# Kernel tuning notes

Measured on AMD Instinct MI355X. Metric: run time of the kernel, lower is better.

The kernel has to match this reference:

```python
import jax, jax.numpy as jnp
import numpy as np

B, C, H, W = 4, 64, 64, 64  # prompt and kv share the same BCHW shape
EPS = 1e-5
OFR = 4.0  # offset_range_factor
SCALE = (C // 1) ** -0.5  # n_head_channels = dim / n_heads = 64


def conv1x1(x, w, b=None):
    y = jnp.einsum('oc,bchw->bohw', w, x)
    if b is not None:
        y = y + b[None, :, None, None]
    return y


def grid_sample_bilinear(img, grid):
    # img: [N,C,Hp,Wp], grid: [N,Hg,Wg,2] with (x,y) in [-1,1], align_corners=True, zeros padding
    N, Cc, Hp, Wp = img.shape
    Hg, Wg = grid.shape[1], grid.shape[2]
    gx = (grid[..., 0] + 1.0) * 0.5 * (Wp - 1)
    gy = (grid[..., 1] + 1.0) * 0.5 * (Hp - 1)
    x0 = jnp.floor(gx)
    y0 = jnp.floor(gy)
    img_f = img.reshape(N, Cc, Hp * Wp)

    def gather(xi, yi):
        valid = (xi >= 0) & (xi <= Wp - 1) & (yi >= 0) & (yi <= Hp - 1)
        xi_c = jnp.clip(xi, 0, Wp - 1).astype(jnp.int32)
        yi_c = jnp.clip(yi, 0, Hp - 1).astype(jnp.int32)
        idx = (yi_c * Wp + xi_c).reshape(N, 1, -1)
        vals = jnp.take_along_axis(img_f, idx, axis=2)  # [N,C,Hg*Wg]
        return vals, valid.reshape(N, 1, -1).astype(img.dtype)

    v00, m00 = gather(x0, y0)
    v01, m01 = gather(x0 + 1, y0)
    v10, m10 = gather(x0, y0 + 1)
    v11, m11 = gather(x0 + 1, y0 + 1)
    wx = (gx - x0).reshape(N, 1, -1)
    wy = (gy - y0).reshape(N, 1, -1)
    out = (v00 * m00 * (1 - wx) * (1 - wy) + v01 * m01 * wx * (1 - wy)
           + v10 * m10 * (1 - wx) * wy + v11 * m11 * wx * wy)
    return out.reshape(N, Cc, Hg, Wg)


def setup_inputs() -> dict:
    key = jax.random.key(0)
    ks = jax.random.split(key, 8)
    s = 0.02
    return {
        'prompt': jax.random.normal(ks[0], (B, C, H, W), jnp.float32),
        'kv': jax.random.normal(ks[1], (B, C, H, W), jnp.float32),
        'wq': s * jax.random.normal(ks[2], (C, C), jnp.float32),
        'bq': jnp.zeros((C,), jnp.float32),
        'wk': s * jax.random.normal(ks[3], (C, C), jnp.float32),
        'bk': jnp.zeros((C,), jnp.float32),
        'wv': s * jax.random.normal(ks[4], (C, C), jnp.float32),
        'bv': jnp.zeros((C,), jnp.float32),
        'wo': s * jax.random.normal(ks[5], (C, C), jnp.float32),
        'bo': jnp.zeros((C,), jnp.float32),
        'dw_w': s * jax.random.normal(ks[6], (C, 1, 3, 3), jnp.float32),  # depthwise 3x3
        'dw_b': jnp.zeros((C,), jnp.float32),
        'ln_w': jnp.ones((C,), jnp.float32),
        'ln_b': jnp.zeros((C,), jnp.float32),
        'off_w': s * jax.random.normal(ks[7], (2, C), jnp.float32),  # 1x1 conv to 2 offset channels
    }


def reference(prompt, kv, wq, bq, wk, bk, wv, bv, wo, bo, dw_w, dw_b, ln_w, ln_b, off_w):
    # q projection (n_groups=1 so group view == full view)
    q = conv1x1(prompt, wq, bq)  # [B,C,H,W]

    # conv_offset: depthwise 3x3 -> WithBias LayerNorm over channels -> GELU -> 1x1 to 2ch
    t = jax.lax.conv_general_dilated(q, dw_w, (1, 1), ((1, 1), (1, 1)),
                                     feature_group_count=C)
    t = t + dw_b[None, :, None, None]
    mu = t.mean(axis=1, keepdims=True)
    var = t.var(axis=1, keepdims=True)
    t = (t - mu) / jnp.sqrt(var + EPS) * ln_w[None, :, None, None] + ln_b[None, :, None, None]
    t = jax.nn.gelu(t, approximate=False)
    offset = jnp.einsum('oc,bchw->bohw', off_w, t)  # [B,2,H,W] (y,x) channels

    Hk, Wk = offset.shape[2], offset.shape[3]
    n = Hk * Wk
    rng = jnp.array([1.0 / (Hk - 1.0), 1.0 / (Wk - 1.0)], dtype=offset.dtype).reshape(1, 2, 1, 1)
    offset = jnp.tanh(offset) * rng * OFR
    offset = jnp.transpose(offset, (0, 2, 3, 1))  # [B,Hk,Wk,2] (y,x)

    ref_y = (jnp.linspace(0.5, Hk - 0.5, Hk) / (Hk - 1.0)) * 2.0 - 1.0
    ref_x = (jnp.linspace(0.5, Wk - 0.5, Wk) / (Wk - 1.0)) * 2.0 - 1.0
    ry, rx = jnp.meshgrid(ref_y, ref_x, indexing='ij')
    ref = jnp.stack((ry, rx), axis=-1)[None].astype(offset.dtype)  # [1,Hk,Wk,2]

    pos = offset + ref
    grid = pos[..., ::-1]  # swap to (x,y)
    xs = grid_sample_bilinear(kv, grid)  # [B,C,Hk,Wk]
    xs = xs.reshape(B, C, n)

    k = jnp.einsum('oc,bcn->bon', wk, xs) + bk[None, :, None]
    v = jnp.einsum('oc,bcn->bon', wv, xs) + bv[None, :, None]
    qf = q.reshape(B, C, H * W)

    attn = jnp.einsum('bcm,bcn->bmn', qf, k) * SCALE  # [B,HW,n]
    attn = jax.nn.softmax(attn, axis=2)
    out = jnp.einsum('bmn,bcn->bcm', attn, v).reshape(B, C, H, W)
    return conv1x1(out, wo, bo)
```

## Files before the change

kernel.cpp:

```cpp
#include <hip/hip_runtime.h>
#include <math.h>

#define BB 4
#define CC 64
#define HH 64
#define WW 64
#define HWP 4096
#define NPTS 4096
#define LDP 72
constexpr float K_EPS   = 1e-5f;
constexpr float K_OFR   = 4.0f;
constexpr float K_QSCALE = 0.18033688011112042f;


typedef short frag8 __attribute__((ext_vector_type(8)));
typedef float f32x4 __attribute__((ext_vector_type(4)));

static __device__ inline unsigned short f2bf(float f) {
  unsigned int u = __builtin_bit_cast(unsigned int, f);
  unsigned int r = (u + 0x7fffu + ((u >> 16) & 1u)) >> 16;
  return (unsigned short)r;
}

#if defined(__has_builtin)
#if __has_builtin(__builtin_amdgcn_cvt_pk_bf16_f32)
#define HAVE_CVT_PK_BF16 1
#endif
#if __has_builtin(__builtin_amdgcn_exp2f)
#define EXP2F(x) __builtin_amdgcn_exp2f(x)
#endif
#endif
#ifndef EXP2F
#define EXP2F(x) exp2f(x)
#endif

static __device__ inline int pack2bf(float a, float b) {
#ifdef HAVE_CVT_PK_BF16
  auto r = __builtin_amdgcn_cvt_pk_bf16_f32(a, b);
  return __builtin_bit_cast(int, r);
#else
  return (int)f2bf(a) | ((int)f2bf(b) << 16);
#endif
}

__global__ __launch_bounds__(1024) void k_qproj(
    const float* __restrict__ prompt, const float* __restrict__ wq,
    const float* __restrict__ bq, float* __restrict__ qf,
    unsigned short* __restrict__ qb) {
  __shared__ float w_s[64 * 64];
  __shared__ float p_s[64 * 64];
  __shared__ unsigned short t_s[64 * 68];
  int tid = threadIdx.x;
  int blk = blockIdx.x;
  int b = blk >> 6; int hw0 = (blk & 63) * 64;
#pragma unroll
  for (int i = 0; i < 4; ++i) w_s[i * 1024 + tid] = wq[i * 1024 + tid];
#pragma unroll
  for (int i = 0; i < 4; ++i) {
    int idx = i * 1024 + tid; int c = idx >> 6, pix = idx & 63;
    p_s[idx] = prompt[(size_t)(b * CC + c) * HWP + hw0 + pix];
  }
  __syncthreads();
  int x = tid & 63, og = tid >> 6;
  float acc[4];
#pragma unroll
  for (int oo = 0; oo < 4; ++oo) acc[oo] = bq[og * 4 + oo];
  for (int cg = 0; cg < 16; ++cg) {
    float p0 = p_s[(cg * 4 + 0) * 64 + x];
    float p1 = p_s[(cg * 4 + 1) * 64 + x];
    float p2 = p_s[(cg * 4 + 2) * 64 + x];
    float p3 = p_s[(cg * 4 + 3) * 64 + x];
#pragma unroll
    for (int oo = 0; oo < 4; ++oo) {
      const float4 w4 = *(const float4*)&w_s[(og * 4 + oo) * 64 + cg * 4];
      acc[oo] = fmaf(w4.x, p0, fmaf(w4.y, p1, fmaf(w4.z, p2, fmaf(w4.w, p3, acc[oo]))));
    }
  }
#pragma unroll
  for (int oo = 0; oo < 4; ++oo) {
    int o = og * 4 + oo;
    qf[(size_t)(b * CC + o) * HWP + hw0 + x] = acc[oo];
    t_s[x * 68 + o] = f2bf(acc[oo] * K_QSCALE);
  }
  __syncthreads();
  {
    int pix = tid >> 4, c4 = tid & 15;
    ushort4 v = *(const ushort4*)&t_s[pix * 68 + c4 * 4];
    *(ushort4*)&qb[(size_t)(b * HWP + hw0 + pix) * CC + c4 * 4] = v;
  }
}

__global__ __launch_bounds__(1024) void k_off_sample(
    const float* __restrict__ q, const float* __restrict__ dw_w,
    const float* __restrict__ dw_b, const float* __restrict__ ln_w,
    const float* __restrict__ ln_b, const float* __restrict__ off_w,
    const float* __restrict__ kv,
    const float* __restrict__ wk, const float* __restrict__ bk,
    const float* __restrict__ wv, const float* __restrict__ bv,
    unsigned short* __restrict__ kb, unsigned short* __restrict__ vb) {
  __shared__ float wk_s[64 * 64];
  __shared__ float wv_s[64 * 64];
  __shared__ float xs_s[64 * 64];
  __shared__ float red0[16][64];
  __shared__ float red1[16][64];

  int tid = threadIdx.x;
  int x = tid & 63;
  int cg = tid >> 6;
  int by = blockIdx.x;
  int b = by >> 6;
  int y = by & 63;

#pragma unroll
  for (int i = 0; i < 4; ++i) {
    wk_s[i * 1024 + tid] = wk[i * 1024 + tid];
    wv_s[i * 1024 + tid] = wv[i * 1024 + tid];
  }

  float t[4];
#pragma unroll
  for (int i = 0; i < 4; ++i) {
    int c = cg * 4 + i;
    float acc = dw_b[c];
    const float* qc = q + (size_t)(b * CC + c) * HWP;
#pragma unroll
    for (int ky = 0; ky < 3; ++ky) {
      int yy = y + ky - 1;
      bool yok = (yy >= 0) && (yy < HH);
#pragma unroll
      for (int kx = 0; kx < 3; ++kx) {
        int xx = x + kx - 1;
        bool ok = yok && (xx >= 0) && (xx < WW);
        float v = ok ? qc[yy * WW + xx] : 0.f;
        acc = fmaf(dw_w[c * 9 + ky * 3 + kx], v, acc);
      }
    }
    t[i] = acc;
  }
  float s1 = 0.f, s2 = 0.f;
#pragma unroll
  for (int i = 0; i < 4; ++i) { s1 += t[i]; s2 += t[i] * t[i]; }
  red0[cg][x] = s1;
  red1[cg][x] = s2;
  __syncthreads();
  float mu = 0.f, ms = 0.f;
#pragma unroll
  for (int g = 0; g < 16; ++g) { mu += red0[g][x]; ms += red1[g][x]; }
  mu *= (1.f / 64.f); ms *= (1.f / 64.f);
  float rstd = rsqrtf(ms - mu * mu + K_EPS);

  float oy = 0.f, ox = 0.f;
#pragma unroll
  for (int i = 0; i < 4; ++i) {
    int c = cg * 4 + i;
    float g = (t[i] - mu) * rstd * ln_w[c] + ln_b[c];
    g = 0.5f * g * (1.f + erff(g * 0.70710678118654752f));
    oy = fmaf(off_w[c], g, oy);
    ox = fmaf(off_w[CC + c], g, ox);
  }
  __syncthreads();
  red0[cg][x] = oy;
  red1[cg][x] = ox;
  __syncthreads();
  if (cg == 0) {
    float osy = 0.f, osx = 0.f;
#pragma unroll
    for (int g = 0; g < 16; ++g) { osy += red0[g][x]; osx += red1[g][x]; }
    osy = tanhf(osy) * (K_OFR / (HH - 1));
    osx = tanhf(osx) * (K_OFR / (WW - 1));
    float ry = (y + 0.5f) * (2.f / 63.f) - 1.f;
    float rx = (x + 0.5f) * (2.f / 63.f) - 1.f;
    red0[0][x] = (osx + rx + 1.f) * 0.5f * (WW - 1);
    red0[1][x] = (osy + ry + 1.f) * 0.5f * (HH - 1);
  }
  __syncthreads();

  int n = x, og = cg;
  int n0 = y * 64;
  float gx = red0[0][n], gy = red0[1][n];
  float x0f = floorf(gx), y0f = floorf(gy);
  float wx = gx - x0f, wy = gy - y0f;
  int x0 = (int)x0f, y0 = (int)y0f;
  int x1 = x0 + 1, y1 = y0 + 1;
  float m00 = (x0 >= 0 && x0 < WW && y0 >= 0 && y0 < HH) ? 1.f : 0.f;
  float m01 = (x1 >= 0 && x1 < WW && y0 >= 0 && y0 < HH) ? 1.f : 0.f;
  float m10 = (x0 >= 0 && x0 < WW && y1 >= 0 && y1 < HH) ? 1.f : 0.f;
  float m11 = (x1 >= 0 && x1 < WW && y1 >= 0 && y1 < HH) ? 1.f : 0.f;
  int x0c = min(max(x0, 0), WW - 1), x1c = min(max(x1, 0), WW - 1);
  int y0c = min(max(y0, 0), HH - 1), y1c = min(max(y1, 0), HH - 1);
  int i00 = y0c * WW + x0c, i01 = y0c * WW + x1c;
  int i10 = y1c * WW + x0c, i11 = y1c * WW + x1c;
  float w00 = m00 * (1.f - wx) * (1.f - wy);
  float w01 = m01 * wx * (1.f - wy);
  float w10 = m10 * (1.f - wx) * wy;
  float w11 = m11 * wx * wy;

  const float* base = kv + (size_t)b * CC * HWP;
#pragma unroll
  for (int i = 0; i < 4; ++i) {
    int c = og * 4 + i;
    const float* pc = base + (size_t)c * HWP;
    xs_s[c * 64 + n] = w00 * pc[i00] + w01 * pc[i01] + w10 * pc[i10] + w11 * pc[i11];
  }
  __syncthreads();
  float ak[4], av[4];
#pragma unroll
  for (int oo = 0; oo < 4; ++oo) { ak[oo] = bk[og * 4 + oo]; av[oo] = bv[og * 4 + oo]; }
  for (int cg2 = 0; cg2 < 16; ++cg2) {
    float p0 = xs_s[(cg2 * 4 + 0) * 64 + n];
    float p1 = xs_s[(cg2 * 4 + 1) * 64 + n];
    float p2 = xs_s[(cg2 * 4 + 2) * 64 + n];
    float p3 = xs_s[(cg2 * 4 + 3) * 64 + n];
#pragma unroll
    for (int oo = 0; oo < 4; ++oo) {
      int o = og * 4 + oo;
      const float4 k4 = *(const float4*)&wk_s[o * 64 + cg2 * 4];
      const float4 v4 = *(const float4*)&wv_s[o * 64 + cg2 * 4];
      ak[oo] = fmaf(k4.x, p0, fmaf(k4.y, p1, fmaf(k4.z, p2, fmaf(k4.w, p3, ak[oo]))));
      av[oo] = fmaf(v4.x, p0, fmaf(v4.y, p1, fmaf(v4.z, p2, fmaf(v4.w, p3, av[oo]))));
    }
  }
  int2 kk;
  kk.x = pack2bf(ak[0], ak[1]);
  kk.y = pack2bf(ak[2], ak[3]);
  size_t krow = (size_t)(b * NPTS + n0 + n) * CC + og * 4;
  *(int2*)&kb[krow] = kk;
#pragma unroll
  for (int oo = 0; oo < 4; ++oo) {
    int o = og * 4 + oo;
    vb[(size_t)(b * CC + o) * NPTS + n0 + n] = f2bf(av[oo]);
  }
}

__global__ __launch_bounds__(256) void k_attn(
    const unsigned short* __restrict__ qb, const unsigned short* __restrict__ kb,
    const unsigned short* __restrict__ vb, float* __restrict__ opart,
    float* __restrict__ dpart, int ns_shift) {
  __shared__ short qp_s[64 * LDP];
  __shared__ short k_s[64 * LDP];
  __shared__ short v_s[64 * LDP];

  int tid = threadIdx.x;
  int w = tid >> 6, lane = tid & 63, quad = lane >> 4, l16 = lane & 15;
  int blk = blockIdx.x;
  int pair = blk & ((BB << ns_shift) - 1);
  int mt = blk >> (2 + ns_shift);
  int ns = pair & ((1 << ns_shift) - 1);
  int b = pair >> ns_shift;
  int m0 = mt * 64;

  const unsigned short* qbb = qb + (size_t)b * HWP * CC;
  const unsigned short* kbb = kb + (size_t)b * NPTS * CC;
  const unsigned short* vbb = vb + (size_t)b * CC * NPTS;

#pragma unroll
  for (int pass = 0; pass < 2; ++pass) {
    int idx = pass * 256 + tid;
    int row = idx >> 3, part = idx & 7;
    uint4 d = *(const uint4*)(qbb + (size_t)(m0 + row) * CC + part * 8);
    *(uint4*)&qp_s[row * LDP + part * 8] = d;
  }
  __syncthreads();
  frag8 a_frag[2];
#pragma unroll
  for (int kc = 0; kc < 2; ++kc)
    a_frag[kc] = *(const frag8*)&qp_s[(w * 16 + l16) * LDP + kc * 32 + quad * 8];

  frag8 ones;
#pragma unroll
  for (int i = 0; i < 8; ++i) ones[i] = (short)0x3F80;

  f32x4 o_acc[4];
  f32x4 d4;
  const f32x4 zz = {0.f, 0.f, 0.f, 0.f};
#pragma unroll
  for (int i = 0; i < 4; ++i) o_acc[i] = zz;
  d4 = zz;

  int niters = (NPTS / 64) >> ns_shift;
  int nbase = ns * niters * 64;
  for (int it = 0; it < niters; ++it) {
    int n0 = nbase + it * 64;
    __syncthreads();
#pragma unroll
    for (int pass = 0; pass < 2; ++pass) {
      int idx = pass * 256 + tid;
      int row = idx >> 3, part = idx & 7;
      uint4 dk = *(const uint4*)(kbb + (size_t)(n0 + row) * CC + part * 8);
      uint4 dv = *(const uint4*)(vbb + (size_t)row * NPTS + n0 + part * 8);
      *(uint4*)&k_s[row * LDP + part * 8] = dk;
      *(uint4*)&v_s[row * LDP + part * 8] = dv;
    }
    __syncthreads();

    f32x4 sT[4];
#pragma unroll
    for (int t = 0; t < 4; ++t) {
      frag8 kf = *(const frag8*)&k_s[(t * 16 + l16) * LDP + quad * 8];
      sT[t] = __builtin_amdgcn_mfma_f32_16x16x32_bf16(kf, a_frag[0], zz, 0, 0, 0);
    }
#pragma unroll
    for (int t = 0; t < 4; ++t) {
      frag8 kf = *(const frag8*)&k_s[(t * 16 + l16) * LDP + 32 + quad * 8];
      sT[t] = __builtin_amdgcn_mfma_f32_16x16x32_bf16(kf, a_frag[1], sT[t], 0, 0, 0);
    }
#pragma unroll
    for (int t = 0; t < 4; ++t) {
      int base_sh = (w * 16 + l16) * LDP + t * 16 + quad * 4;
      int p01 = pack2bf(EXP2F(sT[t][0]), EXP2F(sT[t][1]));
      int p23 = pack2bf(EXP2F(sT[t][2]), EXP2F(sT[t][3]));
      *(int*)&qp_s[base_sh]     = p01;
      *(int*)&qp_s[base_sh + 2] = p23;
    }
#pragma unroll
    for (int kc = 0; kc < 2; ++kc) {
      frag8 bp = *(const frag8*)&qp_s[(w * 16 + l16) * LDP + kc * 32 + quad * 8];
      d4 = __builtin_amdgcn_mfma_f32_16x16x32_bf16(ones, bp, d4, 0, 0, 0);
#pragma unroll
      for (int ct = 0; ct < 4; ++ct) {
        frag8 av = *(const frag8*)&v_s[(ct * 16 + l16) * LDP + kc * 32 + quad * 8];
        o_acc[ct] = __builtin_amdgcn_mfma_f32_16x16x32_bf16(av, bp, o_acc[ct], 0, 0, 0);
      }
    }
  }

  float* op = opart + (size_t)((ns * BB + b) * HWP + m0 + w * 16 + l16) * CC;
#pragma unroll
  for (int ct = 0; ct < 4; ++ct) {
    float4 o4;
    o4.x = o_acc[ct][0]; o4.y = o_acc[ct][1]; o4.z = o_acc[ct][2]; o4.w = o_acc[ct][3];
    *(float4*)&op[ct * 16 + quad * 4] = o4;
  }
  if (lane < 16)
    dpart[(ns * BB + b) * HWP + m0 + w * 16 + lane] = d4[0];
}

__global__ __launch_bounds__(256) void k_out(
    const float* __restrict__ opart, const float* __restrict__ dpart,
    const float* __restrict__ wo, const float* __restrict__ bo,
    float* __restrict__ out, int NS) {
  __shared__ float wo_s[CC * CC];
  __shared__ float t_s[32 * 65];
  int tid = threadIdx.x;
  int blk = blockIdx.x;
  int b = blk >> 7, mt = blk & 127, m0 = mt * 32;
  for (int i = tid; i < CC * CC; i += 256) wo_s[i] = wo[i];

#pragma unroll
  for (int it = 0; it < 8; ++it) {
    int idx = it * 256 + tid;
    int m = idx >> 6, c = idx & 63;
    float o = 0.f, d = 0.f;
    for (int s = 0; s < NS; ++s) {
      o += opart[(size_t)((s * BB + b) * HWP + m0 + m) * CC + c];
      d += dpart[(s * BB + b) * HWP + m0 + m];
    }
    t_s[m * 65 + c] = o / d;
  }
  __syncthreads();
  int ml = tid & 31, og = tid >> 5;
  for (int oo = 0; oo < 8; ++oo) {
    int o = og * 8 + oo;
    float acc = bo[o];
#pragma unroll
    for (int c = 0; c < 64; ++c) acc = fmaf(wo_s[o * CC + c], t_s[ml * 65 + c], acc);
    out[(size_t)(b * CC + o) * HWP + m0 + ml] = acc;
  }
}

extern "C" void kernel_launch(void* const* d_in, const int* in_sizes, int n_in,
                              void* d_out, int out_size, void* d_ws, size_t ws_size,
                              hipStream_t stream) {
  const float* prompt = (const float*)d_in[0];
  const float* kv     = (const float*)d_in[1];
  const float* wq     = (const float*)d_in[2];
  const float* bq     = (const float*)d_in[3];
  const float* wk     = (const float*)d_in[4];
  const float* bk     = (const float*)d_in[5];
  const float* wv     = (const float*)d_in[6];
  const float* bv     = (const float*)d_in[7];
  const float* wo     = (const float*)d_in[8];
  const float* bo     = (const float*)d_in[9];
  const float* dw_w   = (const float*)d_in[10];
  const float* dw_b   = (const float*)d_in[11];
  const float* ln_w   = (const float*)d_in[12];
  const float* ln_b   = (const float*)d_in[13];
  const float* off_w  = (const float*)d_in[14];
  float* out = (float*)d_out;
  float* ws  = (float*)d_ws;

  auto need = [](int ns) {
    return (size_t)((size_t)ns * 1048576 + 3 * 524288 + (size_t)ns * 16384) * sizeof(float);
  };
  int NS, ns_shift;
  if      (ws_size >= need(8)) { NS = 8; ns_shift = 3; }
  else if (ws_size >= need(4)) { NS = 4; ns_shift = 2; }
  else                         { NS = 2; ns_shift = 1; }

  float* opart          = ws;
  float* qf             = ws;
  unsigned short* qb    = (unsigned short*)(ws + (size_t)NS * 1048576);
  unsigned short* kb    = (unsigned short*)(ws + (size_t)NS * 1048576 + 524288);
  unsigned short* vb    = (unsigned short*)(ws + (size_t)NS * 1048576 + 2 * 524288);
  float* dpart          = ws + (size_t)NS * 1048576 + 3 * 524288;

  hipLaunchKernelGGL(k_qproj, dim3(BB * 64), dim3(1024), 0, stream,
                     prompt, wq, bq, qf, qb);
  hipLaunchKernelGGL(k_off_sample, dim3(BB * HH), dim3(1024), 0, stream,
                     qf, dw_w, dw_b, ln_w, ln_b, off_w,
                     kv, wk, bk, wv, bv, kb, vb);
  hipLaunchKernelGGL(k_attn, dim3(BB * NS * 64), dim3(256), 0, stream,
                     qb, kb, vb, opart, dpart, ns_shift);
  hipLaunchKernelGGL(k_out, dim3(BB * 128), dim3(256), 0, stream,
                     opart, dpart, wo, bo, out, NS);
}
```

Measured before the change: 168.8 us.

## Fuse q projection into offset/sampling kernel with halo-row recompute

Merges the q-projection kernel into the offset/sampling kernel. Each block recomputes the q projection for its row plus the two neighbouring rows in shared memory, so the depthwise 3x3 conv reads q from LDS instead of a global fp32 q buffer. This removes one launch and the global round trip of q, at the cost of about three times the q-projection arithmetic and more shared-memory reuse. It also replaces erff in GELU with a polynomial approximation using fast exp2, which lowers precision slightly.

```diff
diff --git a/kernel.cpp b/kernel.cpp
--- a/kernel.cpp
+++ b/kernel.cpp
@@ -43,141 +43,156 @@
 #endif
 }
 
-__global__ __launch_bounds__(1024) void k_qproj(
+static __device__ inline float erf_fast(float z) {
+  float s = (z < 0.f) ? -1.f : 1.f;
+  float a = fabsf(z);
+  float t = 1.f / fmaf(0.3275911f, a, 1.f);
+  float p = t * fmaf(t, fmaf(t, fmaf(t, fmaf(t, 1.061405429f, -1.453152027f),
+                                     1.421413741f), -0.284496736f), 0.254829592f);
+  float e = EXP2F(-a * a * 1.4426950408889634f);
+  return s * (1.f - p * e);
+}
+
+__global__ __launch_bounds__(1024) void k_prep(
     const float* __restrict__ prompt, const float* __restrict__ wq,
-    const float* __restrict__ bq, float* __restrict__ qf,
-    unsigned short* __restrict__ qb) {
-  __shared__ float w_s[64 * 64];
-  __shared__ float p_s[64 * 64];
-  __shared__ unsigned short t_s[64 * 68];
-  int tid = threadIdx.x;
-  int blk = blockIdx.x;
-  int b = blk >> 6; int hw0 = (blk & 63) * 64;
-#pragma unroll
-  for (int i = 0; i < 4; ++i) w_s[i * 1024 + tid] = wq[i * 1024 + tid];
-#pragma unroll
-  for (int i = 0; i < 4; ++i) {
-    int idx = i * 1024 + tid; int c = idx >> 6, pix = idx & 63;
-    p_s[idx] = prompt[(size_t)(b * CC + c) * HWP + hw0 + pix];
-  }
-  __syncthreads();
-  int x = tid & 63, og = tid >> 6;
-  float acc[4];
-#pragma unroll
-  for (int oo = 0; oo < 4; ++oo) acc[oo] = bq[og * 4 + oo];
-  for (int cg = 0; cg < 16; ++cg) {
-    float p0 = p_s[(cg * 4 + 0) * 64 + x];
-    float p1 = p_s[(cg * 4 + 1) * 64 + x];
-    float p2 = p_s[(cg * 4 + 2) * 64 + x];
-    float p3 = p_s[(cg * 4 + 3) * 64 + x];
-#pragma unroll
-    for (int oo = 0; oo < 4; ++oo) {
-      const float4 w4 = *(const float4*)&w_s[(og * 4 + oo) * 64 + cg * 4];
-      acc[oo] = fmaf(w4.x, p0, fmaf(w4.y, p1, fmaf(w4.z, p2, fmaf(w4.w, p3, acc[oo]))));
-    }
-  }
-#pragma unroll
-  for (int oo = 0; oo < 4; ++oo) {
-    int o = og * 4 + oo;
-    qf[(size_t)(b * CC + o) * HWP + hw0 + x] = acc[oo];
-    t_s[x * 68 + o] = f2bf(acc[oo] * K_QSCALE);
-  }
-  __syncthreads();
-  {
-    int pix = tid >> 4, c4 = tid & 15;
-    ushort4 v = *(const ushort4*)&t_s[pix * 68 + c4 * 4];
-    *(ushort4*)&qb[(size_t)(b * HWP + hw0 + pix) * CC + c4 * 4] = v;
-  }
-}
-
-__global__ __launch_bounds__(1024) void k_off_sample(
-    const float* __restrict__ q, const float* __restrict__ dw_w,
-    const float* __restrict__ dw_b, const float* __restrict__ ln_w,
-    const float* __restrict__ ln_b, const float* __restrict__ off_w,
-    const float* __restrict__ kv,
+    const float* __restrict__ bq,
+    const float* __restrict__ dw_w, const float* __restrict__ dw_b,
+    const float* __restrict__ ln_w, const float* __restrict__ ln_b,
+    const float* __restrict__ off_w, const float* __restrict__ kv,
     const float* __restrict__ wk, const float* __restrict__ bk,
     const float* __restrict__ wv, const float* __restrict__ bv,
-    unsigned short* __restrict__ kb, unsigned short* __restrict__ vb) {
-  __shared__ float wk_s[64 * 64];
-  __shared__ float wv_s[64 * 64];
-  __shared__ float xs_s[64 * 64];
-  __shared__ float red0[16][64];
-  __shared__ float red1[16][64];
-
+    unsigned short* __restrict__ qb, unsigned short* __restrict__ kb,
+    unsigned short* __restrict__ vb) {
+  __shared__ float buf[16384];
+  float* w_s = buf;
+  float* pq  = buf + 4096;
   int tid = threadIdx.x;
-  int x = tid & 63;
-  int cg = tid >> 6;
-  int by = blockIdx.x;
-  int b = by >> 6;
-  int y = by & 63;
-
+  int x = tid & 63, og = tid >> 6;
+  int by = blockIdx.x; int b = by >> 6, y = by & 63;
+
+#pragma unroll
+  for (int i = 0; i < 4; ++i) w_s[i * 1024 + tid] = wq[i * 1024 + tid];
+#pragma unroll
+  for (int i = 0; i < 12; ++i) {
+    int idx = i * 1024 + tid;
+    int j = idx >> 6, xx = idx & 63;
+    int c = j / 3, r = j - c * 3;
+    int ry = min(max(y + r - 1, 0), HH - 1);
+    pq[idx] = prompt[(size_t)(b * CC + c) * HWP + ry * WW + xx];
+  }
+  __syncthreads();
+
+  float qreg[3][4];
+#pragma unroll
+  for (int r = 0; r < 3; ++r)
+#pragma unroll
+    for (int oo = 0; oo < 4; ++oo) qreg[r][oo] = bq[og * 4 + oo];
+  for (int cg = 0; cg < 16; ++cg) {
+    float4 w4[4];
+#pragma unroll
+    for (int oo = 0; oo < 4; ++oo)
+      w4[oo] = *(const float4*)&w_s[(og * 4 + oo) * 64 + cg * 4];
+#pragma unroll
+    for (int r = 0; r < 3; ++r) {
+      float p0 = pq[(cg * 4 + 0) * 192 + r * 64 + x];
+      float p1 = pq[(cg * 4 + 1) * 192 + r * 64 + x];
+      float p2 = pq[(cg * 4 + 2) * 192 + r * 64 + x];
+      float p3 = pq[(cg * 4 + 3) * 192 + r * 64 + x];
+#pragma unroll
+      for (int oo = 0; oo < 4; ++oo)
+        qreg[r][oo] = fmaf(w4[oo].x, p0, fmaf(w4[oo].y, p1,
+                      fmaf(w4[oo].z, p2, fmaf(w4[oo].w, p3, qreg[r][oo]))));
+    }
+  }
+  __syncthreads();
+
+#pragma unroll
+  for (int r = 0; r < 3; ++r)
+#pragma unroll
+    for (int oo = 0; oo < 4; ++oo)
+      pq[(og * 4 + oo) * 192 + r * 64 + x] = qreg[r][oo];
+  {
+    int2 qq;
+    qq.x = pack2bf(qreg[1][0] * K_QSCALE, qreg[1][1] * K_QSCALE);
+    qq.y = pack2bf(qreg[1][2] * K_QSCALE, qreg[1][3] * K_QSCALE);
+    *(int2*)&qb[(size_t)(b * HWP + y * WW + x) * CC + og * 4] = qq;
+  }
+  __syncthreads();
+
+  float t[4];
+#pragma unroll
+  for (int i = 0; i < 4; ++i) {
+    int c = og * 4 + i;
+    float acc = dw_b[c];
+#pragma unroll
+    for (int ky = 0; ky < 3; ++ky) {
+      int yy = y + ky - 1;
+      bool yok = (yy >= 0) && (yy < HH);
+#pragma unroll
+      for (int kx = 0; kx < 3; ++kx) {
+        int xx = x + kx - 1;
+        bool ok = yok && (xx >= 0) && (xx < WW);
+        int xc = min(max(xx, 0), WW - 1);
+        float v = ok ? pq[c * 192 + ky * 64 + xc] : 0.f;
+        acc = fmaf(dw_w[c * 9 + ky * 3 + kx], v, acc);
+      }
+    }
+    t[i] = acc;
+  }
+  __syncthreads();
+
+  float* wk_s = pq;
+  float* wv_s = pq + 4096;
+  float* xs_s = pq + 8192;
 #pragma unroll
   for (int i = 0; i < 4; ++i) {
     wk_s[i * 1024 + tid] = wk[i * 1024 + tid];
     wv_s[i * 1024 + tid] = wv[i * 1024 + tid];
   }
 
-  float t[4];
-#pragma unroll
-  for (int i = 0; i < 4; ++i) {
-    int c = cg * 4 + i;
-    float acc = dw_b[c];
-    const float* qc = q + (size_t)(b * CC + c) * HWP;
-#pragma unroll
-    for (int ky = 0; ky < 3; ++ky) {
-      int yy = y + ky - 1;
-      bool yok = (yy >= 0) && (yy < HH);
-#pragma unroll
-      for (int kx = 0; kx < 3; ++kx) {
-        int xx = x + kx - 1;
-        bool ok = yok && (xx >= 0) && (xx < WW);
-        float v = ok ? qc[yy * WW + xx] : 0.f;
-        acc = fmaf(dw_w[c * 9 + ky * 3 + kx], v, acc);
-      }
-    }
-    t[i] = acc;
-  }
+  float* red0 = w_s;
+  float* red1 = w_s + 1024;
   float s1 = 0.f, s2 = 0.f;
 #pragma unroll
   for (int i = 0; i < 4; ++i) { s1 += t[i]; s2 += t[i] * t[i]; }
-  red0[cg][x] = s1;
-  red1[cg][x] = s2;
+  red0[og * 64 + x] = s1;
+  red1[og * 64 + x] = s2;
   __syncthreads();
   float mu = 0.f, ms = 0.f;
 #pragma unroll
-  for (int g = 0; g < 16; ++g) { mu += red0[g][x]; ms += red1[g][x]; }
+  for (int g = 0; g < 16; ++g) { mu += red0[g * 64 + x]; ms += red1[g * 64 + x]; }
   mu *= (1.f / 64.f); ms *= (1.f / 64.f);
   float rstd = rsqrtf(ms - mu * mu + K_EPS);
 
   float oy = 0.f, ox = 0.f;
 #pragma unroll
   for (int i = 0; i < 4; ++i) {
-    int c = cg * 4 + i;
+    int c = og * 4 + i;
     float g = (t[i] - mu) * rstd * ln_w[c] + ln_b[c];
-    g = 0.5f * g * (1.f + erff(g * 0.70710678118654752f));
+    g = 0.5f * g * (1.f + erf_fast(g * 0.70710678118654752f));
     oy = fmaf(off_w[c], g, oy);
     ox = fmaf(off_w[CC + c], g, ox);
   }
   __syncthreads();
-  red0[cg][x] = oy;
-  red1[cg][x] = ox;
-  __syncthreads();
-  if (cg == 0) {
+  red0[og * 64 + x] = oy;
+  red1[og * 64 + x] = ox;
+  __syncthreads();
+  if (og == 0) {
     float osy = 0.f, osx = 0.f;
 #pragma unroll
-    for (int g = 0; g < 16; ++g) { osy += red0[g][x]; osx += red1[g][x]; }
+    for (int g = 0; g < 16; ++g) { osy += red0[g * 64 + x]; osx += red1[g * 64 + x]; }
     osy = tanhf(osy) * (K_OFR / (HH - 1));
     osx = tanhf(osx) * (K_OFR / (WW - 1));
     float ry = (y + 0.5f) * (2.f / 63.f) - 1.f;
     float rx = (x + 0.5f) * (2.f / 63.f) - 1.f;
-    red0[0][x] = (osx + rx + 1.f) * 0.5f * (WW - 1);
-    red0[1][x] = (osy + ry + 1.f) * 0.5f * (HH - 1);
-  }
-  __syncthreads();
-
-  int n = x, og = cg;
+    w_s[2048 + x] = (osx + rx + 1.f) * 0.5f * (WW - 1);
+    w_s[2112 + x] = (osy + ry + 1.f) * 0.5f * (HH - 1);
+  }
+  __syncthreads();
+
+  int n = x;
   int n0 = y * 64;
-  float gx = red0[0][n], gy = red0[1][n];
+  float gx = w_s[2048 + n], gy = w_s[2112 + n];
   float x0f = floorf(gx), y0f = floorf(gy);
   float wx = gx - x0f, wy = gy - y0f;
   int x0 = (int)x0f, y0 = (int)y0f;
@@ -203,6 +218,7 @@
     xs_s[c * 64 + n] = w00 * pc[i00] + w01 * pc[i01] + w10 * pc[i10] + w11 * pc[i11];
   }
   __syncthreads();
+
   float ak[4], av[4];
 #pragma unroll
   for (int oo = 0; oo < 4; ++oo) { ak[oo] = bk[og * 4 + oo]; av[oo] = bv[og * 4 + oo]; }
@@ -223,8 +239,7 @@
   int2 kk;
   kk.x = pack2bf(ak[0], ak[1]);
   kk.y = pack2bf(ak[2], ak[3]);
-  size_t krow = (size_t)(b * NPTS + n0 + n) * CC + og * 4;
-  *(int2*)&kb[krow] = kk;
+  *(int2*)&kb[(size_t)(b * NPTS + n0 + n) * CC + og * 4] = kk;
 #pragma unroll
   for (int oo = 0; oo < 4; ++oo) {
     int o = og * 4 + oo;
@@ -398,17 +413,14 @@
   else                         { NS = 2; ns_shift = 1; }
 
   float* opart          = ws;
-  float* qf             = ws;
   unsigned short* qb    = (unsigned short*)(ws + (size_t)NS * 1048576);
   unsigned short* kb    = (unsigned short*)(ws + (size_t)NS * 1048576 + 524288);
   unsigned short* vb    = (unsigned short*)(ws + (size_t)NS * 1048576 + 2 * 524288);
   float* dpart          = ws + (size_t)NS * 1048576 + 3 * 524288;
 
-  hipLaunchKernelGGL(k_qproj, dim3(BB * 64), dim3(1024), 0, stream,
-                     prompt, wq, bq, qf, qb);
-  hipLaunchKernelGGL(k_off_sample, dim3(BB * HH), dim3(1024), 0, stream,
-                     qf, dw_w, dw_b, ln_w, ln_b, off_w,
-                     kv, wk, bk, wv, bv, kb, vb);
+  hipLaunchKernelGGL(k_prep, dim3(BB * HH), dim3(1024), 0, stream,
+                     prompt, wq, bq, dw_w, dw_b, ln_w, ln_b, off_w,
+                     kv, wk, bk, wv, bv, qb, kb, vb);
   hipLaunchKernelGGL(k_attn, dim3(BB * NS * 64), dim3(256), 0, stream,
                      qb, kb, vb, opart, dpart, ns_shift);
   hipLaunchKernelGGL(k_out, dim3(BB * 128), dim3(256), 0, stream,
```

Result: slower. 173.3 us (+2.7%).

## Swap attention score tiling to hold all Q fragments per wave; use fast erf

Applied to the files above, without the earlier changes.

In the attention kernel, each wave now keeps register fragments for all four 16-row query tiles and loads a single key tile slice. It computes scores for its own 16 keys across all 64 queries and writes exp values into the shared P buffer transposed. An extra block barrier is added before the PV MFMAs, since each wave now reads P rows written by other waves. Separately, erff in the GELU is replaced by an Abramowitz-Stegun polynomial using exp2, trading some accuracy for fewer instructions.

```diff
diff --git a/kernel.cpp b/kernel.cpp
--- a/kernel.cpp
+++ b/kernel.cpp
@@ -41,6 +41,16 @@
 #else
   return (int)f2bf(a) | ((int)f2bf(b) << 16);
 #endif
+}
+
+static __device__ inline float erf_fast(float z) {
+  float s = (z < 0.f) ? -1.f : 1.f;
+  float a = fabsf(z);
+  float t = 1.f / fmaf(0.3275911f, a, 1.f);
+  float p = t * fmaf(t, fmaf(t, fmaf(t, fmaf(t, 1.061405429f, -1.453152027f),
+                                     1.421413741f), -0.284496736f), 0.254829592f);
+  float e = EXP2F(-a * a * 1.4426950408889634f);
+  return s * (1.f - p * e);
 }
 
 __global__ __launch_bounds__(1024) void k_qproj(
@@ -154,7 +164,7 @@
   for (int i = 0; i < 4; ++i) {
     int c = cg * 4 + i;
     float g = (t[i] - mu) * rstd * ln_w[c] + ln_b[c];
-    g = 0.5f * g * (1.f + erff(g * 0.70710678118654752f));
+    g = 0.5f * g * (1.f + erf_fast(g * 0.70710678118654752f));
     oy = fmaf(off_w[c], g, oy);
     ox = fmaf(off_w[CC + c], g, ox);
   }
@@ -223,8 +233,7 @@
   int2 kk;
   kk.x = pack2bf(ak[0], ak[1]);
   kk.y = pack2bf(ak[2], ak[3]);
-  size_t krow = (size_t)(b * NPTS + n0 + n) * CC + og * 4;
-  *(int2*)&kb[krow] = kk;
+  *(int2*)&kb[(size_t)(b * NPTS + n0 + n) * CC + og * 4] = kk;
 #pragma unroll
   for (int oo = 0; oo < 4; ++oo) {
     int o = og * 4 + oo;
@@ -244,10 +253,10 @@
   int w = tid >> 6, lane = tid & 63, quad = lane >> 4, l16 = lane & 15;
   int blk = blockIdx.x;
   int pair = blk & ((BB << ns_shift) - 1);
-  int mt = blk >> (2 + ns_shift);
+  int mtile = blk >> (2 + ns_shift);
   int ns = pair & ((1 << ns_shift) - 1);
   int b = pair >> ns_shift;
-  int m0 = mt * 64;
+  int m0 = mtile * 64;
 
   const unsigned short* qbb = qb + (size_t)b * HWP * CC;
   const unsigned short* kbb = kb + (size_t)b * NPTS * CC;
@@ -261,10 +270,12 @@
     *(uint4*)&qp_s[row * LDP + part * 8] = d;
   }
   __syncthreads();
-  frag8 a_frag[2];
-#pragma unroll
-  for (int kc = 0; kc < 2; ++kc)
-    a_frag[kc] = *(const frag8*)&qp_s[(w * 16 + l16) * LDP + kc * 32 + quad * 8];
+  frag8 qfr[4][2];
+#pragma unroll
+  for (int mt = 0; mt < 4; ++mt)
+#pragma unroll
+    for (int kc = 0; kc < 2; ++kc)
+      qfr[mt][kc] = *(const frag8*)&qp_s[(mt * 16 + l16) * LDP + kc * 32 + quad * 8];
 
   frag8 ones;
 #pragma unroll
@@ -293,25 +304,23 @@
     }
     __syncthreads();
 
+    frag8 kf0 = *(const frag8*)&k_s[(w * 16 + l16) * LDP + quad * 8];
+    frag8 kf1 = *(const frag8*)&k_s[(w * 16 + l16) * LDP + 32 + quad * 8];
     f32x4 sT[4];
 #pragma unroll
-    for (int t = 0; t < 4; ++t) {
-      frag8 kf = *(const frag8*)&k_s[(t * 16 + l16) * LDP + quad * 8];
-      sT[t] = __builtin_amdgcn_mfma_f32_16x16x32_bf16(kf, a_frag[0], zz, 0, 0, 0);
-    }
-#pragma unroll
-    for (int t = 0; t < 4; ++t) {
-      frag8 kf = *(const frag8*)&k_s[(t * 16 + l16) * LDP + 32 + quad * 8];
-      sT[t] = __builtin_amdgcn_mfma_f32_16x16x32_bf16(kf, a_frag[1], sT[t], 0, 0, 0);
-    }
-#pragma unroll
-    for (int t = 0; t < 4; ++t) {
-      int base_sh = (w * 16 + l16) * LDP + t * 16 + quad * 4;
-      int p01 = pack2bf(EXP2F(sT[t][0]), EXP2F(sT[t][1]));
-      int p23 = pack2bf(EXP2F(sT[t][2]), EXP2F(sT[t][3]));
-      *(int*)&qp_s[base_sh]     = p01;
-      *(int*)&qp_s[base_sh + 2] = p23;
-    }
+    for (int mt = 0; mt < 4; ++mt)
+      sT[mt] = __builtin_amdgcn_mfma_f32_16x16x32_bf16(kf0, qfr[mt][0], zz, 0, 0, 0);
+#pragma unroll
+    for (int mt = 0; mt < 4; ++mt)
+      sT[mt] = __builtin_amdgcn_mfma_f32_16x16x32_bf16(kf1, qfr[mt][1], sT[mt], 0, 0, 0);
+#pragma unroll
+    for (int mt = 0; mt < 4; ++mt) {
+      int base_sh = (mt * 16 + l16) * LDP + w * 16 + quad * 4;
+      *(int*)&qp_s[base_sh]     = pack2bf(EXP2F(sT[mt][0]), EXP2F(sT[mt][1]));
+      *(int*)&qp_s[base_sh + 2] = pack2bf(EXP2F(sT[mt][2]), EXP2F(sT[mt][3]));
+    }
+    __syncthreads();
+
 #pragma unroll
     for (int kc = 0; kc < 2; ++kc) {
       frag8 bp = *(const frag8*)&qp_s[(w * 16 + l16) * LDP + kc * 32 + quad * 8];
```

New measurement: 170.0 us. No clear change (+0.7%).

## Enlarge attention query tile to 128 rows with 512 threads; use polynomial erf

Applied to the files above, without the earlier changes.

The attention kernel now processes 128 query rows per block with 8 waves instead of 64 rows with 4 waves. Each K/V tile loaded into shared memory is reused by twice as many queries, which halves global K/V traffic per query, and the grid shrinks accordingly. Separately, the GELU in the offset path swaps erff for an Abramowitz-Stegun polynomial approximation using exp2. That adds some approximation error (around 1e-7) and lowers occupancy per block, in exchange for less load traffic and cheaper transcendental math.

```diff
diff --git a/kernel.cpp b/kernel.cpp
--- a/kernel.cpp
+++ b/kernel.cpp
@@ -41,6 +41,16 @@
 #else
   return (int)f2bf(a) | ((int)f2bf(b) << 16);
 #endif
+}
+
+static __device__ inline float erf_fast(float z) {
+  float s = (z < 0.f) ? -1.f : 1.f;
+  float a = fabsf(z);
+  float t = 1.f / fmaf(0.3275911f, a, 1.f);
+  float p = t * fmaf(t, fmaf(t, fmaf(t, fmaf(t, 1.061405429f, -1.453152027f),
+                                     1.421413741f), -0.284496736f), 0.254829592f);
+  float e = EXP2F(-a * a * 1.4426950408889634f);
+  return s * (1.f - p * e);
 }
 
 __global__ __launch_bounds__(1024) void k_qproj(
@@ -154,7 +164,7 @@
   for (int i = 0; i < 4; ++i) {
     int c = cg * 4 + i;
     float g = (t[i] - mu) * rstd * ln_w[c] + ln_b[c];
-    g = 0.5f * g * (1.f + erff(g * 0.70710678118654752f));
+    g = 0.5f * g * (1.f + erf_fast(g * 0.70710678118654752f));
     oy = fmaf(off_w[c], g, oy);
     ox = fmaf(off_w[CC + c], g, ox);
   }
@@ -223,8 +233,7 @@
   int2 kk;
   kk.x = pack2bf(ak[0], ak[1]);
   kk.y = pack2bf(ak[2], ak[3]);
-  size_t krow = (size_t)(b * NPTS + n0 + n) * CC + og * 4;
-  *(int2*)&kb[krow] = kk;
+  *(int2*)&kb[(size_t)(b * NPTS + n0 + n) * CC + og * 4] = kk;
 #pragma unroll
   for (int oo = 0; oo < 4; ++oo) {
     int o = og * 4 + oo;
@@ -232,11 +241,11 @@
   }
 }
 
-__global__ __launch_bounds__(256) void k_attn(
+__global__ __launch_bounds__(512) void k_attn(
     const unsigned short* __restrict__ qb, const unsigned short* __restrict__ kb,
     const unsigned short* __restrict__ vb, float* __restrict__ opart,
     float* __restrict__ dpart, int ns_shift) {
-  __shared__ short qp_s[64 * LDP];
+  __shared__ short qp_s[128 * LDP];
   __shared__ short k_s[64 * LDP];
   __shared__ short v_s[64 * LDP];
 
@@ -244,10 +253,10 @@
   int w = tid >> 6, lane = tid & 63, quad = lane >> 4, l16 = lane & 15;
   int blk = blockIdx.x;
   int pair = blk & ((BB << ns_shift) - 1);
-  int mt = blk >> (2 + ns_shift);
+  int mtile = blk >> (2 + ns_shift);
   int ns = pair & ((1 << ns_shift) - 1);
   int b = pair >> ns_shift;
-  int m0 = mt * 64;
+  int m0 = mtile * 128;
 
   const unsigned short* qbb = qb + (size_t)b * HWP * CC;
   const unsigned short* kbb = kb + (size_t)b * NPTS * CC;
@@ -255,7 +264,7 @@
 
 #pragma unroll
   for (int pass = 0; pass < 2; ++pass) {
-    int idx = pass * 256 + tid;
+    int idx = pass * 512 + tid;
     int row = idx >> 3, part = idx & 7;
     uint4 d = *(const uint4*)(qbb + (size_t)(m0 + row) * CC + part * 8);
     *(uint4*)&qp_s[row * LDP + part * 8] = d;
@@ -282,10 +291,8 @@
   for (int it = 0; it < niters; ++it) {
     int n0 = nbase + it * 64;
     __syncthreads();
-#pragma unroll
-    for (int pass = 0; pass < 2; ++pass) {
-      int idx = pass * 256 + tid;
-      int row = idx >> 3, part = idx & 7;
+    {
+      int row = tid >> 3, part = tid & 7;
       uint4 dk = *(const uint4*)(kbb + (size_t)(n0 + row) * CC + part * 8);
       uint4 dv = *(const uint4*)(vbb + (size_t)row * NPTS + n0 + part * 8);
       *(uint4*)&k_s[row * LDP + part * 8] = dk;
@@ -307,10 +314,8 @@
 #pragma unroll
     for (int t = 0; t < 4; ++t) {
       int base_sh = (w * 16 + l16) * LDP + t * 16 + quad * 4;
-      int p01 = pack2bf(EXP2F(sT[t][0]), EXP2F(sT[t][1]));
-      int p23 = pack2bf(EXP2F(sT[t][2]), EXP2F(sT[t][3]));
-      *(int*)&qp_s[base_sh]     = p01;
-      *(int*)&qp_s[base_sh + 2] = p23;
+      *(int*)&qp_s[base_sh]     = pack2bf(EXP2F(sT[t][0]), EXP2F(sT[t][1]));
+      *(int*)&qp_s[base_sh + 2] = pack2bf(EXP2F(sT[t][2]), EXP2F(sT[t][3]));
     }
 #pragma unroll
     for (int kc = 0; kc < 2; ++kc) {
@@ -409,7 +414,7 @@
   hipLaunchKernelGGL(k_off_sample, dim3(BB * HH), dim3(1024), 0, stream,
                      qf, dw_w, dw_b, ln_w, ln_b, off_w,
                      kv, wk, bk, wv, bv, kb, vb);
-  hipLaunchKernelGGL(k_attn, dim3(BB * NS * 64), dim3(256), 0, stream,
+  hipLaunchKernelGGL(k_attn, dim3(32 * BB * NS), dim3(512), 0, stream,
                      qb, kb, vb, opart, dpart, ns_shift);
   hipLaunchKernelGGL(k_out, dim3(BB * 128), dim3(256), 0, stream,
                      opart, dpart, wo, bo, out, NS);
```

Result: no change. 167.2 us (-1.0%).
